# Optimization experiments

Hardware: AMD Instinct MI355X
Metric: run time of the kernel (lower is better)

## Reference

```python
import jax, jax.numpy as jnp
import numpy as np

N_EMBD = 1024
N_HEAD = 16
HEAD_DIM = N_EMBD // N_HEAD


def setup_inputs() -> dict:
    key = jax.random.key(0)
    k1, k2, k3, k4, k5 = jax.random.split(key, 5)
    B, T, C = 4, 2048, N_EMBD
    s = 1.0 / np.sqrt(C)
    return {
        "x": jax.random.normal(k1, (B, T, C), dtype=jnp.float32),
        "W_attn": jax.random.normal(k2, (C, 3 * C), dtype=jnp.float32) * s,
        "b_attn": jnp.zeros((3 * C,), dtype=jnp.float32),
        "W_proj": jax.random.normal(k3, (C, C), dtype=jnp.float32) * s,
        "b_proj": jnp.zeros((C,), dtype=jnp.float32),
    }


def reference(x, W_attn, b_attn, W_proj, b_proj):
    B, T, C = x.shape
    H, D = N_HEAD, HEAD_DIM
    # fused QKV projection
    qkv = x @ W_attn + b_attn                       # [B,T,3C]
    q, k, v = jnp.split(qkv, 3, axis=2)
    q = q.reshape(B, T, H, D).transpose(0, 2, 1, 3)  # [B,H,T,D]
    k = k.reshape(B, T, H, D).transpose(0, 2, 1, 3)
    v = v.reshape(B, T, H, D).transpose(0, 2, 1, 3)
    # causal scaled dot-product attention
    scale = 1.0 / jnp.sqrt(jnp.asarray(D, dtype=x.dtype))
    scores = jnp.einsum('bhqd,bhkd->bhqk', q, k) * scale  # [B,H,T,T]
    causal = jnp.tril(jnp.ones((T, T), dtype=bool))
    scores = jnp.where(causal[None, None], scores, jnp.finfo(x.dtype).min)
    attn = jax.nn.softmax(scores, axis=-1)
    y = jnp.einsum('bhqk,bhkd->bhqd', attn, v)      # [B,H,T,D]
    y = y.transpose(0, 2, 1, 3).reshape(B, T, C)
    return y @ W_proj + b_proj
```

## Files before the change

kernel.cpp:

```cpp
#include <hip/hip_runtime.h>
#include <hip/hip_bf16.h>
#include <cstdint>

#define B_ 4
#define T_ 2048
#define C_ 1024
#define H_ 16
#define D_ 64
#define M_ (B_*T_)
#define N3 (3*C_)

typedef __bf16 bf16;
typedef __bf16 bf16x8 __attribute__((ext_vector_type(8)));
typedef __bf16 bf16x4 __attribute__((ext_vector_type(4)));
typedef float  floatx4 __attribute__((ext_vector_type(4)));

__device__ __forceinline__ void gl_lds16(const bf16* g, bf16* l) {
  __builtin_amdgcn_global_load_lds(
      (__attribute__((address_space(1))) void*)(void*)g,
      (__attribute__((address_space(3))) void*)(void*)l,
      16, 0, 0);
}

__device__ __forceinline__ uint32_t pack_bf16_trunc(float lo, float hi) {
  union { float f; uint32_t u; } a, b;
  a.f = lo; b.f = hi;
  return (a.u >> 16) | (b.u & 0xffff0000u);
}

__global__ void cast_to_bf16(const float* __restrict__ in, bf16* __restrict__ out, int n) {
  int i = (blockIdx.x * blockDim.x + threadIdx.x) * 4;
  if (i < n) {
    const float4 f = *(const float4*)(in + i);
    bf16x4 o;
    o.x = (bf16)f.x; o.y = (bf16)f.y; o.z = (bf16)f.z; o.w = (bf16)f.w;
    *(bf16x4*)(out + i) = o;
  }
}

__global__ void transpose_cast(const float* __restrict__ in, bf16* __restrict__ out,
                               int R, int C) {
  __shared__ float tile[32][33];
  int r0 = blockIdx.y * 32, c0 = blockIdx.x * 32;
  int tx = threadIdx.x & 31, ty = threadIdx.x >> 5;
  #pragma unroll
  for (int j = 0; j < 32; j += 8)
    tile[ty + j][tx] = in[(size_t)(r0 + ty + j) * C + c0 + tx];
  __syncthreads();
  #pragma unroll
  for (int j = 0; j < 32; j += 8)
    out[(size_t)(c0 + ty + j) * R + r0 + tx] = (bf16)tile[tx][ty + j];
}

__global__ __launch_bounds__(256)
void transpose_v(const bf16* __restrict__ in, bf16* __restrict__ out) {
  __shared__ __attribute__((aligned(16))) bf16 tileN[64 * 64];
  const int tid = threadIdx.x;
  const int bh = blockIdx.z;
  const int t0 = blockIdx.x * 64;
  const int sk = tid >> 2, scc = tid & 3;
  {
    const bf16* p = in + ((size_t)bh * T_ + t0 + sk) * D_ + scc * 16;
    const bf16x8 r0 = *(const bf16x8*)p;
    const bf16x8 r1 = *(const bf16x8*)(p + 8);
    *(bf16x8*)(tileN + sk * 64 + ((2 * scc)     ^ (sk & 7)) * 8) = r0;
    *(bf16x8*)(tileN + sk * 64 + ((2 * scc + 1) ^ (sk & 7)) * 8) = r1;
  }
  __syncthreads();
  const int tc = (tid & 7) * 8;
  #pragma unroll
  for (int half = 0; half < 2; half++) {
    const int d = (tid >> 3) + half * 32;
    bf16x8 o;
    #pragma unroll
    for (int j = 0; j < 8; j++) {
      const int slot = tc + j;
      const int row = 16 * (slot & 3) + (slot >> 2);
      o[j] = tileN[row * 64 + (((d >> 3) ^ (row & 7)) * 8) + (d & 7)];
    }
    *(bf16x8*)(out + ((size_t)bh * D_ + d) * T_ + t0 + tc) = o;
  }
}

template<int MODE>
__global__ __launch_bounds__(256)
void gemm_bt(const bf16* __restrict__ A, const bf16* __restrict__ Bt,
             const float* __restrict__ bias, float* __restrict__ out,
             bf16* __restrict__ qo, bf16* __restrict__ ko, bf16* __restrict__ vo,
             int M, int N, int K)
{
  __shared__ __attribute__((aligned(16))) bf16 As[128 * 32];
  __shared__ __attribute__((aligned(16))) bf16 Bs[128 * 32];

  const int tid  = threadIdx.x;
  const int w    = tid >> 6;
  const int lane = tid & 63;
  const int quad = lane >> 4;
  const int l16  = lane & 15;
  const int wm   = w & 1, wn = w >> 1;
  const int m0   = blockIdx.y * 128, n0 = blockIdx.x * 128;

  floatx4 acc[4][4] = {};

  const int lrow = lane >> 2;
  const int lk   = (lane & 3) * 8;

  const bf16* aptr = A  + (size_t)(m0 + w * 32 + lrow) * K + lk;
  const bf16* bptr = Bt + (size_t)(n0 + w * 32 + lrow) * K + lk;
  bf16* asl = As + w * 1024;
  bf16* bsl = Bs + w * 1024;

  for (int k0 = 0; k0 < K; k0 += 32) {
    gl_lds16(aptr,          asl);
    gl_lds16(aptr + 16 * K, asl + 512);
    gl_lds16(bptr,          bsl);
    gl_lds16(bptr + 16 * K, bsl + 512);
    aptr += 32; bptr += 32;
    __syncthreads();

    bf16x8 af[4], bfb[4];
    #pragma unroll
    for (int i = 0; i < 4; i++)
      af[i] = *(const bf16x8*)(As + (wm * 64 + i * 16 + l16) * 32 + quad * 8);
    #pragma unroll
    for (int i = 0; i < 4; i++)
      bfb[i] = *(const bf16x8*)(Bs + (wn * 64 + i * 16 + l16) * 32 + quad * 8);
    #pragma unroll
    for (int mi = 0; mi < 4; mi++)
      #pragma unroll
      for (int ni = 0; ni < 4; ni++)
        acc[mi][ni] = __builtin_amdgcn_mfma_f32_16x16x32_bf16(af[mi], bfb[ni], acc[mi][ni], 0, 0, 0);
    __syncthreads();
  }

  #pragma unroll
  for (int mi = 0; mi < 4; mi++) {
    #pragma unroll
    for (int ni = 0; ni < 4; ni++) {
      const int col = n0 + wn * 64 + ni * 16 + l16;
      const float bv = bias[col];
      #pragma unroll
      for (int r = 0; r < 4; r++) {
        const int row = m0 + wm * 64 + mi * 16 + quad * 4 + r;
        const float val = acc[mi][ni][r] + bv;
        if (MODE == 0) {
          const int b = row >> 11, t = row & 2047;
          const int s = col >> 10, c = col & 1023;
          const int h = c >> 6,  d = c & 63;
          bf16* dst = (s == 0) ? qo : (s == 1) ? ko : vo;
          dst[((size_t)(b * H_ + h) * T_ + t) * D_ + d] = (bf16)val;
        } else {
          out[(size_t)row * N + col] = val;
        }
      }
    }
  }
}

__global__ __launch_bounds__(256)
void attn_kernel(const bf16* __restrict__ Q, const bf16* __restrict__ Kp,
                 const bf16* __restrict__ Vtp, bf16* __restrict__ Y)
{
  __shared__ __attribute__((aligned(16))) bf16 Ks[2][64 * 72];
  __shared__ __attribute__((aligned(16))) bf16 Vs[2][64 * 72];
  __shared__ __attribute__((aligned(16))) bf16 Ps[4][16 * 72];

  const int tid  = threadIdx.x;
  const int w    = tid >> 6, lane = tid & 63;
  const int quad = lane >> 4, l16 = lane & 15;
  const int bh = blockIdx.x;
  const int b = bh >> 4, h = bh & 15;
  const int pr = blockIdx.y;

  const int sk = tid >> 2;
  const int sc = (tid & 3) * 16;

  const float SC = 0.125f * 1.44269504088896f;

  #pragma unroll 1
  for (int sel = 0; sel < 2; sel++) {
    const int qt = sel ? pr : 15 - pr;
    const int q0 = qt * 128;
    const int nch = 2 * qt + 2;

    bf16x8 qf[2][2];
    #pragma unroll
    for (int mt = 0; mt < 2; mt++) {
      const bf16* qp = Q + ((size_t)bh * T_ + q0 + mt * 64 + w * 16 + l16) * D_ + quad * 8;
      qf[mt][0] = *(const bf16x8*)qp;
      qf[mt][1] = *(const bf16x8*)(qp + 32);
    }

    floatx4 o[2][4] = {};
    float l_r[2][4] = {};

    const bf16* kpp = Kp  + (size_t)bh * T_ * D_ + (size_t)sk * D_ + sc;
    const bf16* vpp = Vtp + (size_t)bh * D_ * T_ + (size_t)sk * T_ + sc;

    {
      const bf16x8 k0 = *(const bf16x8*)kpp, k1 = *(const bf16x8*)(kpp + 8);
      const bf16x8 v0 = *(const bf16x8*)vpp, v1 = *(const bf16x8*)(vpp + 8);
      bf16* kd = Ks[0] + sk * 72 + sc;
      *(bf16x8*)kd = k0; *(bf16x8*)(kd + 8) = k1;
      bf16* vd = Vs[0] + sk * 72 + sc;
      *(bf16x8*)vd = v0; *(bf16x8*)(vd + 8) = v1;
      kpp += 64 * D_; vpp += 64;
    }
    __syncthreads();

    #pragma unroll 1
    for (int c = 0; c < nch; c++) {
      const int cur = c & 1;

      bf16x8 nk0, nk1, nv0, nv1;
      const bool have = (c + 1 < nch);
      if (have) {
        nk0 = *(const bf16x8*)kpp; nk1 = *(const bf16x8*)(kpp + 8);
        nv0 = *(const bf16x8*)vpp; nv1 = *(const bf16x8*)(vpp + 8);
        kpp += 64 * D_; vpp += 64;
      }

      const bf16* KsC = Ks[cur];
      const bf16* VsC = Vs[cur];
      const int kv0 = c * 64;
      const bool act0 = (c < nch - 1);

      floatx4 s[2][4];
      #pragma unroll
      for (int nt = 0; nt < 4; nt++) {
        const bf16x8 kf0 = *(const bf16x8*)(KsC + (nt * 16 + l16) * 72 + quad * 8);
        const bf16x8 kf1 = *(const bf16x8*)(KsC + (nt * 16 + l16) * 72 + 32 + quad * 8);
        if (act0) {
          floatx4 z = {};
          z = __builtin_amdgcn_mfma_f32_16x16x32_bf16(qf[0][0], kf0, z, 0, 0, 0);
          s[0][nt] = __builtin_amdgcn_mfma_f32_16x16x32_bf16(qf[0][1], kf1, z, 0, 0, 0);
        }
        floatx4 z = {};
        z = __builtin_amdgcn_mfma_f32_16x16x32_bf16(qf[1][0], kf0, z, 0, 0, 0);
        s[1][nt] = __builtin_amdgcn_mfma_f32_16x16x32_bf16(qf[1][1], kf1, z, 0, 0, 0);
      }

      bf16x8 vfr[4][2];
      #pragma unroll
      for (int nt = 0; nt < 4; nt++) {
        vfr[nt][0] = *(const bf16x8*)(VsC + (nt * 16 + l16) * 72 + quad * 8);
        vfr[nt][1] = *(const bf16x8*)(VsC + (nt * 16 + l16) * 72 + 32 + quad * 8);
      }

      #pragma unroll
      for (int mt = 0; mt < 2; mt++) {
        if (mt == 0 && !act0) continue;
        const bool diag = (c == 2 * qt + mt);
        #pragma unroll
        for (int r = 0; r < 4; r++) {
          const int qrow = q0 + mt * 64 + w * 16 + quad * 4 + r;
          float x0 = s[mt][0][r], x1 = s[mt][1][r], x2 = s[mt][2][r], x3 = s[mt][3][r];
          if (diag) {
            if (kv0      + l16 > qrow) x0 = -1e30f;
            if (kv0 + 16 + l16 > qrow) x1 = -1e30f;
            if (kv0 + 32 + l16 > qrow) x2 = -1e30f;
            if (kv0 + 48 + l16 > qrow) x3 = -1e30f;
          }
          const float e0 = __builtin_amdgcn_exp2f(fmaf(x0, SC, -8.f));
          const float e1 = __builtin_amdgcn_exp2f(fmaf(x1, SC, -8.f));
          const float e2 = __builtin_amdgcn_exp2f(fmaf(x2, SC, -8.f));
          const float e3 = __builtin_amdgcn_exp2f(fmaf(x3, SC, -8.f));
          l_r[mt][r] += (e0 + e1) + (e2 + e3);
          uint2 pk;
          pk.x = pack_bf16_trunc(e0, e1);
          pk.y = pack_bf16_trunc(e2, e3);
          *(uint2*)(&Ps[w][(quad * 4 + r) * 72 + l16 * 4]) = pk;
        }
        const bf16x8 pf0 = *(const bf16x8*)(&Ps[w][l16 * 72 + quad * 8]);
        const bf16x8 pf1 = *(const bf16x8*)(&Ps[w][l16 * 72 + 32 + quad * 8]);
        #pragma unroll
        for (int nt = 0; nt < 4; nt++) {
          o[mt][nt] = __builtin_amdgcn_mfma_f32_16x16x32_bf16(pf0, vfr[nt][0], o[mt][nt], 0, 0, 0);
          o[mt][nt] = __builtin_amdgcn_mfma_f32_16x16x32_bf16(pf1, vfr[nt][1], o[mt][nt], 0, 0, 0);
        }
      }

      if (have) {
        bf16* kd = Ks[cur ^ 1] + sk * 72 + sc;
        *(bf16x8*)kd = nk0; *(bf16x8*)(kd + 8) = nk1;
        bf16* vd = Vs[cur ^ 1] + sk * 72 + sc;
        *(bf16x8*)vd = nv0; *(bf16x8*)(vd + 8) = nv1;
      }
      __syncthreads();
    }

    #pragma unroll
    for (int mt = 0; mt < 2; mt++) {
      #pragma unroll
      for (int r = 0; r < 4; r++) {
        float ls = l_r[mt][r];
        ls += __shfl_xor(ls, 1);
        ls += __shfl_xor(ls, 2);
        ls += __shfl_xor(ls, 4);
        ls += __shfl_xor(ls, 8);
        const float inv = 1.f / ls;
        const int t = q0 + mt * 64 + w * 16 + quad * 4 + r;
        #pragma unroll
        for (int nt = 0; nt < 4; nt++)
          Y[((size_t)b * T_ + t) * C_ + h * D_ + nt * 16 + l16] = (bf16)(o[mt][nt][r] * inv);
      }
    }
  }
}

extern "C" void kernel_launch(void* const* d_in, const int* in_sizes, int n_in,
                              void* d_out, int out_size, void* d_ws, size_t ws_size,
                              hipStream_t stream)
{
  const float* x      = (const float*)d_in[0];
  const float* W_attn = (const float*)d_in[1];
  const float* b_attn = (const float*)d_in[2];
  const float* W_proj = (const float*)d_in[3];
  const float* b_proj = (const float*)d_in[4];
  float* out = (float*)d_out;

  bf16* xb  = (bf16*)d_ws;
  bf16* wat = xb  + (size_t)M_ * C_;
  bf16* wpt = wat + (size_t)N3 * C_;
  bf16* qb  = wpt + (size_t)C_ * C_;
  bf16* kb  = qb  + (size_t)M_ * C_;
  bf16* vb  = kb  + (size_t)M_ * C_;
  bf16* yb  = vb  + (size_t)M_ * C_;
  bf16* vtb = xb;

  cast_to_bf16<<<dim3(M_ * C_ / 1024), 256, 0, stream>>>(x, xb, M_ * C_);
  transpose_cast<<<dim3(N3 / 32, C_ / 32), 256, 0, stream>>>(W_attn, wat, C_, N3);
  transpose_cast<<<dim3(C_ / 32, C_ / 32), 256, 0, stream>>>(W_proj, wpt, C_, C_);
  gemm_bt<0><<<dim3(N3 / 128, M_ / 128), 256, 0, stream>>>(
      xb, wat, b_attn, nullptr, qb, kb, vb, M_, N3, C_);
  transpose_v<<<dim3(T_ / 64, 1, B_ * H_), 256, 0, stream>>>(vb, vtb);
  attn_kernel<<<dim3(B_ * H_, 8), 256, 0, stream>>>(qb, kb, vtb, yb);
  gemm_bt<1><<<dim3(C_ / 128, M_ / 128), 256, 0, stream>>>(
      yb, wpt, b_proj, out, nullptr, nullptr, nullptr, M_, C_, C_);
}
```

Measured before the change: 269.7 us.

## Use 256x256-tile 512-thread pipelined GEMM for QKV projection

Adds a new GEMM kernel with 256x256 output tiles, 8 waves, XOR-swizzled LDS staging through global_load_lds, and staggered half-tile prefetch interleaved with MFMA phases under setprio. The QKV projection launch now uses it in place of the 128x128 kernel. The aim is more data reuse per LDS load and overlap of global loads with compute. In exchange it uses 128KB of LDS and a large accumulator register footprint, which may limit occupancy, and the grid is only 12x32 blocks.

```diff
diff --git a/kernel.cpp b/kernel.cpp
--- a/kernel.cpp
+++ b/kernel.cpp
@@ -149,6 +149,148 @@
           const int h = c >> 6,  d = c & 63;
           bf16* dst = (s == 0) ? qo : (s == 1) ? ko : vo;
           dst[((size_t)(b * H_ + h) * T_ + t) * D_ + d] = (bf16)val;
+        } else {
+          out[(size_t)row * N + col] = val;
+        }
+      }
+    }
+  }
+}
+
+
+__device__ __forceinline__ void stage8(const bf16* g, int K, bf16* lds, int lane) {
+  const int r = lane >> 3, s = (lane & 7) ^ r;
+  gl_lds16(g + (size_t)r * K + s * 8, lds);
+}
+__device__ __forceinline__ void stage_half(const bf16* g, int K, bf16* lds, int wv, int lane) {
+  stage8(g + (size_t)(wv * 16) * K,     K, lds + (wv * 16) * 64, lane);
+  stage8(g + (size_t)(wv * 16 + 8) * K, K, lds + (wv * 16 + 8) * 64, lane);
+}
+
+#define GBAR asm volatile("s_barrier" ::: "memory")
+
+template<int MODE>
+__global__ __launch_bounds__(512, 2)
+void gemm256(const bf16* __restrict__ A, const bf16* __restrict__ Bt,
+             const float* __restrict__ bias, float* __restrict__ out,
+             bf16* __restrict__ qo, bf16* __restrict__ ko, bf16* __restrict__ vo,
+             int M, int N, int K)
+{
+  __shared__ __attribute__((aligned(16))) bf16 As[2][256 * 64];
+  __shared__ __attribute__((aligned(16))) bf16 Bs[2][256 * 64];
+
+  const int tid  = threadIdx.x;
+  const int wv   = tid >> 6, lane = tid & 63;
+  const int quad = lane >> 4, l16 = lane & 15;
+  const int wm   = wv >> 2, wn = wv & 3;
+  const int n0   = blockIdx.x * 256, m0 = blockIdx.y * 256;
+  const int NTT  = K >> 6;
+
+  floatx4 acc[8][4] = {};
+
+  const bf16* Abase = A  + (size_t)m0 * K;
+  const bf16* Bbase = Bt + (size_t)n0 * K;
+
+  stage_half(Abase,                  K, As[0],            wv, lane);
+  stage_half(Abase + (size_t)128*K,  K, As[0] + 128 * 64, wv, lane);
+  stage_half(Bbase,                  K, Bs[0],            wv, lane);
+  stage_half(Bbase + (size_t)128*K,  K, Bs[0] + 128 * 64, wv, lane);
+  stage_half(Abase + 64,             K, As[1],            wv, lane);
+  stage_half(Bbase + 64,             K, Bs[1],            wv, lane);
+  asm volatile("s_waitcnt vmcnt(4)" ::: "memory");
+  GBAR;
+
+#define LOADA(qm)                                                          \
+  _Pragma("unroll")                                                        \
+  for (int mi = 0; mi < 4; mi++) {                                         \
+    const int row = wm * 128 + (qm) * 64 + mi * 16 + l16;                  \
+    const bf16* rp = bufA + row * 64;                                      \
+    af[mi][0] = *(const bf16x8*)(rp + (( quad      ^ (row & 7)) * 8));     \
+    af[mi][1] = *(const bf16x8*)(rp + (((4 | quad) ^ (row & 7)) * 8));     \
+  }
+#define LOADB(qn)                                                          \
+  _Pragma("unroll")                                                        \
+  for (int ni = 0; ni < 2; ni++) {                                         \
+    const int row = wn * 64 + (qn) * 32 + ni * 16 + l16;                   \
+    const bf16* rp = bufB + row * 64;                                      \
+    bfr[ni][0] = *(const bf16x8*)(rp + (( quad      ^ (row & 7)) * 8));    \
+    bfr[ni][1] = *(const bf16x8*)(rp + (((4 | quad) ^ (row & 7)) * 8));    \
+  }
+#define MM(qm, qn)                                                         \
+  __builtin_amdgcn_s_setprio(1);                                           \
+  _Pragma("unroll")                                                        \
+  for (int mi = 0; mi < 4; mi++)                                           \
+    _Pragma("unroll")                                                      \
+    for (int ni = 0; ni < 2; ni++) {                                       \
+      acc[(qm)*4+mi][(qn)*2+ni] = __builtin_amdgcn_mfma_f32_16x16x32_bf16( \
+          af[mi][0], bfr[ni][0], acc[(qm)*4+mi][(qn)*2+ni], 0, 0, 0);      \
+      acc[(qm)*4+mi][(qn)*2+ni] = __builtin_amdgcn_mfma_f32_16x16x32_bf16( \
+          af[mi][1], bfr[ni][1], acc[(qm)*4+mi][(qn)*2+ni], 0, 0, 0);      \
+    }                                                                      \
+  __builtin_amdgcn_s_setprio(0);
+
+  #pragma unroll 1
+  for (int t = 0; t < NTT; t++) {
+    const int cur = t & 1;
+    const bf16* bufA = As[cur];
+    const bf16* bufB = Bs[cur];
+    bf16* nA = As[cur ^ 1];
+    bf16* nB = Bs[cur ^ 1];
+    bf16* cA = As[cur];
+    bf16* cB = Bs[cur];
+    const int kn1 = (t + 1) * 64, kn2 = (t + 2) * 64;
+    const bool h1 = (t + 1 < NTT), h2 = (t + 2 < NTT);
+
+    bf16x8 af[4][2], bfr[2][2];
+
+    LOADA(0);
+    LOADB(0);
+    if (h1) stage_half(Abase + (size_t)128 * K + kn1, K, nA + 128 * 64, wv, lane);
+    GBAR;
+    MM(0, 0);
+    GBAR;
+
+    LOADB(1);
+    if (h1) stage_half(Bbase + (size_t)128 * K + kn1, K, nB + 128 * 64, wv, lane);
+    GBAR;
+    MM(0, 1);
+    GBAR;
+
+    LOADA(1);
+    LOADB(0);
+    if (h2) stage_half(Abase + kn2, K, cA, wv, lane);
+    GBAR;
+    MM(1, 0);
+    GBAR;
+
+    LOADB(1);
+    if (h2) stage_half(Bbase + kn2, K, cB, wv, lane);
+    GBAR;
+    MM(1, 1);
+    asm volatile("s_waitcnt vmcnt(4)" ::: "memory");
+    GBAR;
+  }
+
+#undef LOADA
+#undef LOADB
+#undef MM
+
+  #pragma unroll
+  for (int mi8 = 0; mi8 < 8; mi8++) {
+    #pragma unroll
+    for (int nf = 0; nf < 4; nf++) {
+      const int col = n0 + wn * 64 + nf * 16 + l16;
+      const float bv = bias[col];
+      #pragma unroll
+      for (int r = 0; r < 4; r++) {
+        const int row = m0 + wm * 128 + mi8 * 16 + quad * 4 + r;
+        const float val = acc[mi8][nf][r] + bv;
+        if (MODE == 0) {
+          const int b = row >> 11, tt = row & 2047;
+          const int s = col >> 10, c = col & 1023;
+          const int h = c >> 6, d = c & 63;
+          bf16* dst = (s == 0) ? qo : (s == 1) ? ko : vo;
+          dst[((size_t)(b * H_ + h) * T_ + tt) * D_ + d] = (bf16)val;
         } else {
           out[(size_t)row * N + col] = val;
         }
@@ -331,7 +473,7 @@
   cast_to_bf16<<<dim3(M_ * C_ / 1024), 256, 0, stream>>>(x, xb, M_ * C_);
   transpose_cast<<<dim3(N3 / 32, C_ / 32), 256, 0, stream>>>(W_attn, wat, C_, N3);
   transpose_cast<<<dim3(C_ / 32, C_ / 32), 256, 0, stream>>>(W_proj, wpt, C_, C_);
-  gemm_bt<0><<<dim3(N3 / 128, M_ / 128), 256, 0, stream>>>(
+  gemm256<0><<<dim3(N3 / 256, M_ / 256), 512, 0, stream>>>(
       xb, wat, b_attn, nullptr, qb, kb, vb, M_, N3, C_);
   transpose_v<<<dim3(T_ / 64, 1, B_ * H_), 256, 0, stream>>>(vb, vtb);
   attn_kernel<<<dim3(B_ * H_, 8), 256, 0, stream>>>(qb, kb, vtb, yb);
```

New measurement: 272.9 us. About the same (+1.2%).
